# Kernel optimization log

Hardware: AMD Instinct MI355X
Metric: run time of the kernel (lower is better)

## Reference

```python
import jax, jax.numpy as jnp
import numpy as np

DIM = 1024
NUM_HEADS = 16
HEAD_DIM = DIM // NUM_HEADS
MAX_LEN = 2048
ROPE_BASE = 10000.0


def _rope_tables(n, d, base=ROPE_BASE):
    inv_freq = 1.0 / (base ** (np.arange(0, d, 2, dtype=np.float32) / d))  # [d/2]
    t = np.arange(n, dtype=np.float32)
    freqs = np.outer(t, inv_freq)  # [n, d/2]
    return jnp.asarray(np.cos(freqs)), jnp.asarray(np.sin(freqs))


def _apply_rotary(x, cos, sin):
    # x: [B, H, N, D]; pairs are consecutive elements (2i, 2i+1)
    xe = x[..., 0::2]
    xo = x[..., 1::2]
    # cos/sin: [N, D/2] -> broadcast over B, H
    oe = xe * cos - xo * sin
    oo = xe * sin + xo * cos
    return jnp.stack([oe, oo], axis=-1).reshape(x.shape)


def setup_inputs() -> dict:
    key = jax.random.key(0)
    ks = jax.random.split(key, 11)
    B, T, S = 4, 2048, 2048
    sc = 1.0 / np.sqrt(DIM)
    inp = {
        "query": jax.random.normal(ks[0], (B, T, DIM), jnp.float32),
        "key": jax.random.normal(ks[1], (B, S, DIM), jnp.float32),
        "value": jax.random.normal(ks[2], (B, S, DIM), jnp.float32),
        "Wq": jax.random.normal(ks[3], (DIM, DIM), jnp.float32) * sc,
        "bq": jnp.zeros((DIM,), jnp.float32),
        "Wk": jax.random.normal(ks[4], (DIM, DIM), jnp.float32) * sc,
        "bk": jnp.zeros((DIM,), jnp.float32),
        "Wv": jax.random.normal(ks[5], (DIM, DIM), jnp.float32) * sc,
        "bv": jnp.zeros((DIM,), jnp.float32),
        "Wo": jax.random.normal(ks[6], (DIM, DIM), jnp.float32) * sc,
        "bo": jnp.zeros((DIM,), jnp.float32),
    }
    return inp


def reference(query, key, value, Wq, bq, Wk, bk, Wv, bv, Wo, bo):
    B, T, C = query.shape
    S = key.shape[1]
    H, D = NUM_HEADS, HEAD_DIM
    scale = D ** -0.5

    q = (query @ Wq + bq).reshape(B, T, H, D).transpose(0, 2, 1, 3)  # [B,H,T,D]
    k = (key @ Wk + bk).reshape(B, S, H, D).transpose(0, 2, 1, 3)    # [B,H,S,D]
    v = (value @ Wv + bv).reshape(B, S, H, D).transpose(0, 2, 1, 3)  # [B,H,S,D]

    cos, sin = _rope_tables(max(T, S), D)
    q = _apply_rotary(q, cos[:T], sin[:T])
    k = _apply_rotary(k, cos[:S], sin[:S])

    scores = jnp.einsum("bhtd,bhsd->bhts", q, k) * scale  # [B,H,T,S]
    causal = jnp.tril(jnp.ones((T, S), bool))
    scores = jnp.where(causal[None, None], scores, -jnp.inf)
    att = jax.nn.softmax(scores, axis=-1)

    out = jnp.einsum("bhts,bhsd->bhtd", att, v)  # [B,H,T,D]
    out = out.transpose(0, 2, 1, 3).reshape(B, T, C)
    return out @ Wo + bo
```

## Files before the change

kernel.cpp:

```cpp
#include <hip/hip_runtime.h>
#include <cstdint>
#include <math.h>

typedef __bf16 bf16_t;
typedef __bf16 bf16x8 __attribute__((ext_vector_type(8)));
typedef float f32x4 __attribute__((ext_vector_type(4)));

#define MFMA16(a, b, c) __builtin_amdgcn_mfma_f32_16x16x32_bf16((a), (b), (c), 0, 0, 0)

static constexpr int BATCH = 4;
static constexpr int SEQ = 2048;
static constexpr int DIMC = 1024;
static constexpr int NH = 16;
static constexpr int HD = 64;

__device__ __forceinline__ void async_copy16(void* lds, const void* g) {
    __builtin_amdgcn_global_load_lds(
        (const __attribute__((address_space(1))) void*)g,
        (__attribute__((address_space(3))) void*)lds, 16, 0, 0);
}

__device__ __forceinline__ float fast_exp2(float x) {
#if __has_builtin(__builtin_amdgcn_exp2f)
    return __builtin_amdgcn_exp2f(x);
#else
    return __expf(x * 0.6931471805599453f);
#endif
}

__global__ __launch_bounds__(256) void cvt_bf16(const float* __restrict__ in,
                                                bf16_t* __restrict__ out) {
    const int i = blockIdx.x * 256 + threadIdx.x;
    const float4 f0 = ((const float4*)in)[i * 2];
    const float4 f1 = ((const float4*)in)[i * 2 + 1];
    bf16x8 v;
    v[0] = (bf16_t)f0.x; v[1] = (bf16_t)f0.y; v[2] = (bf16_t)f0.z; v[3] = (bf16_t)f0.w;
    v[4] = (bf16_t)f1.x; v[5] = (bf16_t)f1.y; v[6] = (bf16_t)f1.z; v[7] = (bf16_t)f1.w;
    ((bf16x8*)out)[i] = v;
}

__global__ __launch_bounds__(256) void transpose_cvt(const float* __restrict__ W0,
                                                     const float* __restrict__ W1,
                                                     const float* __restrict__ W2,
                                                     const float* __restrict__ W3,
                                                     bf16_t* __restrict__ out) {
    const float* Ws[4] = {W0, W1, W2, W3};
    const float* W = Ws[blockIdx.z];
    bf16_t* Wt = out + (size_t)blockIdx.z * DIMC * DIMC;
    __shared__ float tile[32][33];
    const int tx = threadIdx.x & 31;
    const int ty = threadIdx.x >> 5;
    const int x0 = blockIdx.x * 32;
    const int y0 = blockIdx.y * 32;
    #pragma unroll
    for (int j = ty; j < 32; j += 8)
        tile[j][tx] = W[(size_t)(y0 + j) * DIMC + x0 + tx];
    __syncthreads();
    #pragma unroll
    for (int j = ty; j < 32; j += 8)
        Wt[(size_t)(x0 + j) * DIMC + y0 + tx] = (bf16_t)tile[tx][j];
}

__global__ __launch_bounds__(256) void rope_tab(float* __restrict__ cosT, float* __restrict__ sinT) {
    const int idx = blockIdx.x * 256 + threadIdx.x;
    const int t = idx >> 5;
    const int p = idx & 31;
    const float inv = exp2f(-0.41524101186092029f * (float)p);
    const float ang = (float)t * inv;
    float s, c;
    sincosf(ang, &s, &c);
    cosT[idx] = c;
    sinT[idx] = s;
}

template <int MODE>
__global__ __launch_bounds__(256) void gemm_kernel(const bf16_t* __restrict__ A,
                                                   const bf16_t* __restrict__ Bt,
                                                   const float* __restrict__ bias,
                                                   void* __restrict__ outv,
                                                   const float* __restrict__ cosT,
                                                   const float* __restrict__ sinT) {
    constexpr int K = DIMC;
    __shared__ bf16_t As[128 * 32];
    __shared__ bf16_t Bs[128 * 32];
    const int tid = threadIdx.x;
    const int w = tid >> 6;
    const int lane = tid & 63;
    const int l15 = lane & 15;
    const int quad = lane >> 4;
    const int wr = w >> 1, wc = w & 1;
    const int row0 = blockIdx.y * 128, col0 = blockIdx.x * 128;
    f32x4 acc[4][4] = {};
    for (int kt = 0; kt < K / 32; ++kt) {
        const int k0 = kt * 32;
        __syncthreads();
        #pragma unroll
        for (int ci = 0; ci < 2; ++ci) {
            const int c = 2 * w + ci;
            async_copy16(&Bs[c * 512],
                         Bt + (size_t)(col0 + c * 16 + (lane >> 2)) * K + k0 + (lane & 3) * 8);
            async_copy16(&As[c * 512],
                         A + (size_t)(row0 + c * 16 + (lane >> 2)) * K + k0 + (lane & 3) * 8);
        }
        __syncthreads();
        bf16x8 af[4], bfr[4];
        #pragma unroll
        for (int mt = 0; mt < 4; ++mt)
            af[mt] = *(const bf16x8*)&As[(wr * 64 + mt * 16 + l15) * 32 + quad * 8];
        #pragma unroll
        for (int nt = 0; nt < 4; ++nt)
            bfr[nt] = *(const bf16x8*)&Bs[(wc * 64 + nt * 16 + l15) * 32 + quad * 8];
        #pragma unroll
        for (int mt = 0; mt < 4; ++mt)
            #pragma unroll
            for (int nt = 0; nt < 4; ++nt)
                acc[mt][nt] = MFMA16(af[mt], bfr[nt], acc[mt][nt]);
    }
    #pragma unroll
    for (int nt = 0; nt < 4; ++nt) {
        const int col = col0 + wc * 64 + nt * 16 + l15;
        const float bv = bias[col];
        #pragma unroll
        for (int mt = 0; mt < 4; ++mt) {
            #pragma unroll
            for (int r = 0; r < 4; ++r) {
                const int row = row0 + wr * 64 + mt * 16 + quad * 4 + r;
                float v = acc[mt][nt][r] + bv;
                if constexpr (MODE == 2) {
                    ((float*)outv)[(size_t)row * DIMC + col] = v;
                } else {
                    const int t = row & (SEQ - 1);
                    const int bb = row >> 11;
                    const int h = col >> 6;
                    const int d = col & 63;
                    float o = v;
                    if constexpr (MODE == 0) {
                        const int p = d >> 1;
                        const float cs = cosT[t * 32 + p];
                        const float sn = sinT[t * 32 + p];
                        const float partner = __shfl_xor(v, 1);
                        o = (d & 1) ? (partner * sn + v * cs) : (v * cs - partner * sn);
                    }
                    ((bf16_t*)outv)[(((size_t)bb * NH + h) * SEQ + t) * HD + d] = (bf16_t)o;
                }
            }
        }
    }
}

__global__ __launch_bounds__(256) void attn_kernel(const bf16_t* __restrict__ Qr,
                                                   const bf16_t* __restrict__ Kr,
                                                   const bf16_t* __restrict__ Vr,
                                                   bf16_t* __restrict__ O) {
    __shared__ bf16_t Ks[64 * 72];
    __shared__ bf16_t Vt[64 * 72];
    __shared__ bf16_t Ps[4][32 * 72];
    const int tid = threadIdx.x;
    const int w = tid >> 6;
    const int lane = tid & 63;
    const int l15 = lane & 15;
    const int quad = lane >> 4;
    const int bh = blockIdx.y;
    const int b = bh >> 4, h = bh & 15;
    const bf16_t* Qb = Qr + (size_t)bh * SEQ * HD;
    const bf16_t* Kb = Kr + (size_t)bh * SEQ * HD;
    const bf16_t* Vb = Vr + (size_t)bh * SEQ * HD;
    const float S2 = 0.18033688011112043f;

    bf16x8 ones;
    #pragma unroll
    for (int j8 = 0; j8 < 8; ++j8) ones[j8] = (bf16_t)1.0f;

    for (int half = 0; half < 2; ++half) {
        const int j = (half == 0) ? blockIdx.x : 15 - blockIdx.x;
        const int q0 = j * 128;
        bf16x8 qa[2][2];
        #pragma unroll
        for (int mg = 0; mg < 2; ++mg)
            #pragma unroll
            for (int kc = 0; kc < 2; ++kc)
                qa[mg][kc] = *(const bf16x8*)(Qb + (size_t)(q0 + mg * 64 + w * 16 + l15) * HD +
                                              kc * 32 + quad * 8);
        f32x4 acco[2][4] = {};
        f32x4 accl[2] = {};
        const int nIter = 2 * j + 2;
        for (int it = 0; it < nIter; ++it) {
            const int s0 = it * 64;
            __syncthreads();
            {
                const int s = tid >> 2, c4 = tid & 3;
                const bf16_t* src = Kb + (size_t)(s0 + s) * HD + c4 * 16;
                bf16x8 k0 = *(const bf16x8*)src;
                bf16x8 k1 = *(const bf16x8*)(src + 8);
                *(bf16x8*)&Ks[s * 72 + c4 * 16] = k0;
                *(bf16x8*)&Ks[s * 72 + c4 * 16 + 8] = k1;
            }
            #pragma unroll
            for (int cc = 0; cc < 2; ++cc) {
                const int d0 = w * 8 + cc * 32;
                const int s = lane;
                bf16x8 vv = *(const bf16x8*)(Vb + (size_t)(s0 + s) * HD + d0);
                #pragma unroll
                for (int j8 = 0; j8 < 8; ++j8) Vt[(d0 + j8) * 72 + s] = vv[j8];
            }
            __syncthreads();
            bf16x8 kb[4][2];
            #pragma unroll
            for (int nt = 0; nt < 4; ++nt) {
                kb[nt][0] = *(const bf16x8*)&Ks[(nt * 16 + l15) * 72 + quad * 8];
                kb[nt][1] = *(const bf16x8*)&Ks[(nt * 16 + l15) * 72 + 32 + quad * 8];
            }
            #pragma unroll
            for (int mg = 0; mg < 2; ++mg) {
                if (mg == 0 && it == 2 * j + 1) continue;
                f32x4 sc[4];
                #pragma unroll
                for (int nt = 0; nt < 4; ++nt) {
                    f32x4 z = {};
                    z = MFMA16(qa[mg][0], kb[nt][0], z);
                    z = MFMA16(qa[mg][1], kb[nt][1], z);
                    sc[nt] = z;
                }
                const bool diag = (it == 2 * j + mg);
                #pragma unroll
                for (int nt = 0; nt < 4; ++nt) {
                    #pragma unroll
                    for (int r = 0; r < 4; ++r) {
                        float v = sc[nt][r];
                        if (diag) {
                            const int lcol = nt * 16 + l15;
                            const int lrow = w * 16 + quad * 4 + r;
                            if (lcol > lrow) v = -INFINITY;
                        }
                        const float p = fast_exp2(S2 * v);
                        Ps[w][(mg * 16 + quad * 4 + r) * 72 + nt * 16 + l15] = (bf16_t)p;
                    }
                }
            }
            asm volatile("s_waitcnt lgkmcnt(0)" ::: "memory");
            bf16x8 vb[4][2];
            #pragma unroll
            for (int dt = 0; dt < 4; ++dt) {
                vb[dt][0] = *(const bf16x8*)&Vt[(dt * 16 + l15) * 72 + quad * 8];
                vb[dt][1] = *(const bf16x8*)&Vt[(dt * 16 + l15) * 72 + 32 + quad * 8];
            }
            #pragma unroll
            for (int mg = 0; mg < 2; ++mg) {
                if (mg == 0 && it == 2 * j + 1) continue;
                const bf16x8 pa0 = *(const bf16x8*)&Ps[w][(mg * 16 + l15) * 72 + quad * 8];
                const bf16x8 pa1 = *(const bf16x8*)&Ps[w][(mg * 16 + l15) * 72 + 32 + quad * 8];
                #pragma unroll
                for (int dt = 0; dt < 4; ++dt) {
                    acco[mg][dt] = MFMA16(pa0, vb[dt][0], acco[mg][dt]);
                    acco[mg][dt] = MFMA16(pa1, vb[dt][1], acco[mg][dt]);
                }
                accl[mg] = MFMA16(pa0, ones, accl[mg]);
                accl[mg] = MFMA16(pa1, ones, accl[mg]);
            }
        }
        #pragma unroll
        for (int mg = 0; mg < 2; ++mg) {
            #pragma unroll
            for (int r = 0; r < 4; ++r) {
                const float inv = 1.0f / accl[mg][r];
                const int trow = q0 + mg * 64 + w * 16 + quad * 4 + r;
                bf16_t* orow = O + ((size_t)(b * SEQ + trow)) * DIMC + h * HD;
                #pragma unroll
                for (int dt = 0; dt < 4; ++dt)
                    orow[dt * 16 + l15] = (bf16_t)(acco[mg][dt][r] * inv);
            }
        }
    }
}

extern "C" void kernel_launch(void* const* d_in, const int* in_sizes, int n_in,
                              void* d_out, int out_size, void* d_ws, size_t ws_size,
                              hipStream_t stream) {
    const float* query = (const float*)d_in[0];
    const float* key = (const float*)d_in[1];
    const float* value = (const float*)d_in[2];
    const float* Wq = (const float*)d_in[3];
    const float* bq = (const float*)d_in[4];
    const float* Wk = (const float*)d_in[5];
    const float* bk = (const float*)d_in[6];
    const float* Wv = (const float*)d_in[7];
    const float* bv = (const float*)d_in[8];
    const float* Wo = (const float*)d_in[9];
    const float* bo = (const float*)d_in[10];

    char* ws = (char*)d_ws;
    const size_t WT_BYTES = (size_t)DIMC * DIMC * sizeof(bf16_t);
    bf16_t* WqT = (bf16_t*)ws;
    bf16_t* WkT = WqT + (size_t)DIMC * DIMC;
    bf16_t* WvT = WqT + 2 * (size_t)DIMC * DIMC;
    bf16_t* WoT = WqT + 3 * (size_t)DIMC * DIMC;
    float* cosT = (float*)(ws + 4 * WT_BYTES);
    float* sinT = (float*)(ws + 4 * WT_BYTES + 262144);
    char* p = ws + 4 * WT_BYTES + 2 * 262144;
    const size_t ACT_BYTES = (size_t)BATCH * SEQ * DIMC * sizeof(bf16_t);
    bf16_t* Qr = (bf16_t*)(p);
    bf16_t* Kr = (bf16_t*)(p + ACT_BYTES);
    bf16_t* Vr = (bf16_t*)(p + 2 * ACT_BYTES);
    bf16_t* Ob = (bf16_t*)(p + 3 * ACT_BYTES);

    transpose_cvt<<<dim3(32, 32, 4), 256, 0, stream>>>(Wq, Wk, Wv, Wo, (bf16_t*)ws);
    rope_tab<<<dim3(256), 256, 0, stream>>>(cosT, sinT);

    const int cvt_blocks = (BATCH * SEQ * DIMC) / (8 * 256);
    dim3 gg(DIMC / 128, (BATCH * SEQ) / 128);

    cvt_bf16<<<dim3(cvt_blocks), 256, 0, stream>>>(query, Ob);
    gemm_kernel<0><<<gg, 256, 0, stream>>>(Ob, WqT, bq, Qr, cosT, sinT);
    cvt_bf16<<<dim3(cvt_blocks), 256, 0, stream>>>(key, Ob);
    gemm_kernel<0><<<gg, 256, 0, stream>>>(Ob, WkT, bk, Kr, cosT, sinT);
    cvt_bf16<<<dim3(cvt_blocks), 256, 0, stream>>>(value, Ob);
    gemm_kernel<1><<<gg, 256, 0, stream>>>(Ob, WvT, bv, Vr, cosT, sinT);

    attn_kernel<<<dim3(8, BATCH * NH), 256, 0, stream>>>(Qr, Kr, Vr, Ob);
    gemm_kernel<2><<<gg, 256, 0, stream>>>(Ob, WoT, bo, d_out, nullptr, nullptr);
}
```

Measured before the change: 374.9 us.

## Batch QKV projections, swizzle GEMM LDS, async K loads and MFMA-based V transpose

The three input conversions and three projection GEMMs are merged into single launches over a z grid dimension, so there are fewer launches and each wave is larger. GEMM LDS tiles use an XOR swizzle to cut bank conflicts on fragment reads. In attention, K tiles are loaded with async global-to-LDS copies into a swizzled unpadded buffer. V is transposed through an identity-matrix MFMA instead of scalar LDS scatter, and the score MFMA operands are swapped so P can be stored as packed 4-wide vectors. These changes trade more complex indexing and extra MFMA work for fewer launches and less LDS traffic.

Result: no change. 372.6 us (-0.6%).

```diff
diff --git a/kernel.cpp b/kernel.cpp
--- a/kernel.cpp
+++ b/kernel.cpp
@@ -4,6 +4,7 @@
 
 typedef __bf16 bf16_t;
 typedef __bf16 bf16x8 __attribute__((ext_vector_type(8)));
+typedef __bf16 bf16x4 __attribute__((ext_vector_type(4)));
 typedef float f32x4 __attribute__((ext_vector_type(4)));
 
 #define MFMA16(a, b, c) __builtin_amdgcn_mfma_f32_16x16x32_bf16((a), (b), (c), 0, 0, 0)
@@ -28,15 +29,19 @@
 #endif
 }
 
-__global__ __launch_bounds__(256) void cvt_bf16(const float* __restrict__ in,
-                                                bf16_t* __restrict__ out) {
+__global__ __launch_bounds__(256) void cvt3(const float* __restrict__ q,
+                                            const float* __restrict__ k,
+                                            const float* __restrict__ v,
+                                            bf16_t* __restrict__ out) {
+    const float* in = (blockIdx.y == 0) ? q : ((blockIdx.y == 1) ? k : v);
+    bf16_t* o = out + (size_t)blockIdx.y * BATCH * SEQ * DIMC;
     const int i = blockIdx.x * 256 + threadIdx.x;
     const float4 f0 = ((const float4*)in)[i * 2];
     const float4 f1 = ((const float4*)in)[i * 2 + 1];
-    bf16x8 v;
-    v[0] = (bf16_t)f0.x; v[1] = (bf16_t)f0.y; v[2] = (bf16_t)f0.z; v[3] = (bf16_t)f0.w;
-    v[4] = (bf16_t)f1.x; v[5] = (bf16_t)f1.y; v[6] = (bf16_t)f1.z; v[7] = (bf16_t)f1.w;
-    ((bf16x8*)out)[i] = v;
+    bf16x8 vv;
+    vv[0] = (bf16_t)f0.x; vv[1] = (bf16_t)f0.y; vv[2] = (bf16_t)f0.z; vv[3] = (bf16_t)f0.w;
+    vv[4] = (bf16_t)f1.x; vv[5] = (bf16_t)f1.y; vv[6] = (bf16_t)f1.z; vv[7] = (bf16_t)f1.w;
+    ((bf16x8*)o)[i] = vv;
 }
 
 __global__ __launch_bounds__(256) void transpose_cvt(const float* __restrict__ W0,
@@ -73,14 +78,89 @@
     sinT[idx] = s;
 }
 
-template <int MODE>
-__global__ __launch_bounds__(256) void gemm_kernel(const bf16_t* __restrict__ A,
-                                                   const bf16_t* __restrict__ Bt,
-                                                   const float* __restrict__ bias,
-                                                   void* __restrict__ outv,
-                                                   const float* __restrict__ cosT,
-                                                   const float* __restrict__ sinT) {
-    constexpr int K = DIMC;
+#define GEMM_KLOOP(A_, Bt_)                                                             \
+    f32x4 acc[4][4] = {};                                                               \
+    const int swW = ((lane >> 2) & 3) ^ ((lane >> 4) & 3);         \
+    const int rIn = lane >> 2;                                    \
+    const int gW = ((lane & 3) ^ swW) * 8;                        \
+    const int fR = (l15 & 3) ^ ((l15 >> 2) & 3);                    \
+    for (int kt = 0; kt < DIMC / 32; ++kt) {                                            \
+        const int k0 = kt * 32;                                                         \
+        __syncthreads();                                                                \
+        _Pragma("unroll") for (int ci = 0; ci < 2; ++ci) {                              \
+            const int c = 2 * w + ci;                                                   \
+            async_copy16(&Bs[c * 512], Bt_ + (size_t)(col0 + c * 16 + rIn) * DIMC + k0 + gW); \
+            async_copy16(&As[c * 512], A_ + (size_t)(row0 + c * 16 + rIn) * DIMC + k0 + gW);  \
+        }                                                                               \
+        __syncthreads();                                                                \
+        bf16x8 af[4], bfr[4];                                                           \
+        _Pragma("unroll") for (int mt = 0; mt < 4; ++mt)                                \
+            af[mt] = *(const bf16x8*)&As[(wr * 64 + mt * 16 + l15) * 32 + ((quad ^ fR) << 3)]; \
+        _Pragma("unroll") for (int nt = 0; nt < 4; ++nt)                                \
+            bfr[nt] = *(const bf16x8*)&Bs[(wc * 64 + nt * 16 + l15) * 32 + ((quad ^ fR) << 3)]; \
+        _Pragma("unroll") for (int mt = 0; mt < 4; ++mt)                                \
+            _Pragma("unroll") for (int nt = 0; nt < 4; ++nt)                            \
+                acc[mt][nt] = MFMA16(af[mt], bfr[nt], acc[mt][nt]);                     \
+    }
+
+__global__ __launch_bounds__(256) void gemm_qkv(const bf16_t* __restrict__ Cb,
+                                                const bf16_t* __restrict__ Wt3,
+                                                const float* __restrict__ bq,
+                                                const float* __restrict__ bk,
+                                                const float* __restrict__ bv,
+                                                bf16_t* __restrict__ Qr,
+                                                bf16_t* __restrict__ Kr,
+                                                bf16_t* __restrict__ Vr,
+                                                const float* __restrict__ cosT,
+                                                const float* __restrict__ sinT) {
+    __shared__ bf16_t As[128 * 32];
+    __shared__ bf16_t Bs[128 * 32];
+    const int z = blockIdx.z;
+    const bf16_t* A = Cb + (size_t)z * BATCH * SEQ * DIMC;
+    const bf16_t* Bt = Wt3 + (size_t)z * DIMC * DIMC;
+    const float* bias = (z == 0) ? bq : ((z == 1) ? bk : bv);
+    bf16_t* outp = (z == 0) ? Qr : ((z == 1) ? Kr : Vr);
+    const bool rope = (z < 2);
+    const int tid = threadIdx.x;
+    const int w = tid >> 6;
+    const int lane = tid & 63;
+    const int l15 = lane & 15;
+    const int quad = lane >> 4;
+    const int wr = w >> 1, wc = w & 1;
+    const int row0 = blockIdx.y * 128, col0 = blockIdx.x * 128;
+    GEMM_KLOOP(A, Bt)
+    #pragma unroll
+    for (int nt = 0; nt < 4; ++nt) {
+        const int col = col0 + wc * 64 + nt * 16 + l15;
+        const float bvl = bias[col];
+        const int h = col >> 6;
+        const int d = col & 63;
+        #pragma unroll
+        for (int mt = 0; mt < 4; ++mt) {
+            #pragma unroll
+            for (int r = 0; r < 4; ++r) {
+                const int row = row0 + wr * 64 + mt * 16 + quad * 4 + r;
+                const int t = row & (SEQ - 1);
+                const int bb = row >> 11;
+                float v = acc[mt][nt][r] + bvl;
+                float o = v;
+                if (rope) {
+                    const int p = d >> 1;
+                    const float cs = cosT[t * 32 + p];
+                    const float sn = sinT[t * 32 + p];
+                    const float partner = __shfl_xor(v, 1);
+                    o = (d & 1) ? (partner * sn + v * cs) : (v * cs - partner * sn);
+                }
+                outp[(((size_t)bb * NH + h) * SEQ + t) * HD + d] = (bf16_t)o;
+            }
+        }
+    }
+}
+
+__global__ __launch_bounds__(256) void gemm_o(const bf16_t* __restrict__ A,
+                                              const bf16_t* __restrict__ Bt,
+                                              const float* __restrict__ bias,
+                                              float* __restrict__ out) {
     __shared__ bf16_t As[128 * 32];
     __shared__ bf16_t Bs[128 * 32];
     const int tid = threadIdx.x;
@@ -90,59 +170,17 @@
     const int quad = lane >> 4;
     const int wr = w >> 1, wc = w & 1;
     const int row0 = blockIdx.y * 128, col0 = blockIdx.x * 128;
-    f32x4 acc[4][4] = {};
-    for (int kt = 0; kt < K / 32; ++kt) {
-        const int k0 = kt * 32;
-        __syncthreads();
-        #pragma unroll
-        for (int ci = 0; ci < 2; ++ci) {
-            const int c = 2 * w + ci;
-            async_copy16(&Bs[c * 512],
-                         Bt + (size_t)(col0 + c * 16 + (lane >> 2)) * K + k0 + (lane & 3) * 8);
-            async_copy16(&As[c * 512],
-                         A + (size_t)(row0 + c * 16 + (lane >> 2)) * K + k0 + (lane & 3) * 8);
-        }
-        __syncthreads();
-        bf16x8 af[4], bfr[4];
-        #pragma unroll
-        for (int mt = 0; mt < 4; ++mt)
-            af[mt] = *(const bf16x8*)&As[(wr * 64 + mt * 16 + l15) * 32 + quad * 8];
-        #pragma unroll
-        for (int nt = 0; nt < 4; ++nt)
-            bfr[nt] = *(const bf16x8*)&Bs[(wc * 64 + nt * 16 + l15) * 32 + quad * 8];
-        #pragma unroll
-        for (int mt = 0; mt < 4; ++mt)
-            #pragma unroll
-            for (int nt = 0; nt < 4; ++nt)
-                acc[mt][nt] = MFMA16(af[mt], bfr[nt], acc[mt][nt]);
-    }
+    GEMM_KLOOP(A, Bt)
     #pragma unroll
     for (int nt = 0; nt < 4; ++nt) {
         const int col = col0 + wc * 64 + nt * 16 + l15;
-        const float bv = bias[col];
+        const float bvl = bias[col];
         #pragma unroll
         for (int mt = 0; mt < 4; ++mt) {
             #pragma unroll
             for (int r = 0; r < 4; ++r) {
                 const int row = row0 + wr * 64 + mt * 16 + quad * 4 + r;
-                float v = acc[mt][nt][r] + bv;
-                if constexpr (MODE == 2) {
-                    ((float*)outv)[(size_t)row * DIMC + col] = v;
-                } else {
-                    const int t = row & (SEQ - 1);
-                    const int bb = row >> 11;
-                    const int h = col >> 6;
-                    const int d = col & 63;
-                    float o = v;
-                    if constexpr (MODE == 0) {
-                        const int p = d >> 1;
-                        const float cs = cosT[t * 32 + p];
-                        const float sn = sinT[t * 32 + p];
-                        const float partner = __shfl_xor(v, 1);
-                        o = (d & 1) ? (partner * sn + v * cs) : (v * cs - partner * sn);
-                    }
-                    ((bf16_t*)outv)[(((size_t)bb * NH + h) * SEQ + t) * HD + d] = (bf16_t)o;
-                }
+                out[(size_t)row * DIMC + col] = acc[mt][nt][r] + bvl;
             }
         }
     }
@@ -152,7 +190,7 @@
                                                    const bf16_t* __restrict__ Kr,
                                                    const bf16_t* __restrict__ Vr,
                                                    bf16_t* __restrict__ O) {
-    __shared__ bf16_t Ks[64 * 72];
+    __shared__ bf16_t Ks[64 * 64];
     __shared__ bf16_t Vt[64 * 72];
     __shared__ bf16_t Ps[4][32 * 72];
     const int tid = threadIdx.x;
@@ -170,6 +208,16 @@
     bf16x8 ones;
     #pragma unroll
     for (int j8 = 0; j8 < 8; ++j8) ones[j8] = (bf16_t)1.0f;
+    bf16x8 idB[2];
+    #pragma unroll
+    for (int ch = 0; ch < 2; ++ch)
+        #pragma unroll
+        for (int j8 = 0; j8 < 8; ++j8)
+            idB[ch][j8] = (quad * 8 + j8 == ch * 16 + l15) ? (bf16_t)1.0f : (bf16_t)0.0f;
+
+    const int sIn = lane >> 3;
+    const int gK = ((lane & 7) ^ sIn) * 8;
+    const int fK = (l15 & 7);
 
     for (int half = 0; half < 2; ++half) {
         const int j = (half == 0) ? blockIdx.x : 15 - blockIdx.x;
@@ -187,63 +235,59 @@
         for (int it = 0; it < nIter; ++it) {
             const int s0 = it * 64;
             __syncthreads();
+            #pragma unroll
+            for (int ci = 0; ci < 2; ++ci) {
+                const int c = 2 * w + ci;
+                async_copy16(&Ks[c * 512], Kb + (size_t)(s0 + c * 8 + sIn) * HD + gK);
+            }
             {
-                const int s = tid >> 2, c4 = tid & 3;
-                const bf16_t* src = Kb + (size_t)(s0 + s) * HD + c4 * 16;
-                bf16x8 k0 = *(const bf16x8*)src;
-                bf16x8 k1 = *(const bf16x8*)(src + 8);
-                *(bf16x8*)&Ks[s * 72 + c4 * 16] = k0;
-                *(bf16x8*)&Ks[s * 72 + c4 * 16 + 8] = k1;
-            }
-            #pragma unroll
-            for (int cc = 0; cc < 2; ++cc) {
-                const int d0 = w * 8 + cc * 32;
-                const int s = lane;
-                bf16x8 vv = *(const bf16x8*)(Vb + (size_t)(s0 + s) * HD + d0);
-                #pragma unroll
-                for (int j8 = 0; j8 < 8; ++j8) Vt[(d0 + j8) * 72 + s] = vv[j8];
+                const bf16_t* vsrc = Vb + (size_t)(s0 + w * 16 + l15) * HD + quad * 8;
+                bf16x8 av0 = *(const bf16x8*)(vsrc);
+                bf16x8 av1 = *(const bf16x8*)(vsrc + 32);
+                #pragma unroll
+                for (int c = 0; c < 4; ++c) {
+                    f32x4 zz = {};
+                    f32x4 tv = MFMA16((c < 2) ? av0 : av1, idB[c & 1], zz);
+                    bf16x4 pk;
+                    #pragma unroll
+                    for (int r = 0; r < 4; ++r) pk[r] = (bf16_t)tv[r];
+                    *(bf16x4*)&Vt[(c * 16 + l15) * 72 + w * 16 + quad * 4] = pk;
+                }
             }
             __syncthreads();
             bf16x8 kb[4][2];
             #pragma unroll
-            for (int nt = 0; nt < 4; ++nt) {
-                kb[nt][0] = *(const bf16x8*)&Ks[(nt * 16 + l15) * 72 + quad * 8];
-                kb[nt][1] = *(const bf16x8*)&Ks[(nt * 16 + l15) * 72 + 32 + quad * 8];
-            }
+            for (int mt = 0; mt < 4; ++mt)
+                #pragma unroll
+                for (int kc = 0; kc < 2; ++kc)
+                    kb[mt][kc] = *(const bf16x8*)&Ks[(mt * 16 + l15) * 64 +
+                                                     (((kc * 4 + quad) ^ fK) << 3)];
             #pragma unroll
             for (int mg = 0; mg < 2; ++mg) {
                 if (mg == 0 && it == 2 * j + 1) continue;
-                f32x4 sc[4];
-                #pragma unroll
-                for (int nt = 0; nt < 4; ++nt) {
+                const bool diag = (it == 2 * j + mg);
+                #pragma unroll
+                for (int mt = 0; mt < 4; ++mt) {
                     f32x4 z = {};
-                    z = MFMA16(qa[mg][0], kb[nt][0], z);
-                    z = MFMA16(qa[mg][1], kb[nt][1], z);
-                    sc[nt] = z;
-                }
-                const bool diag = (it == 2 * j + mg);
-                #pragma unroll
-                for (int nt = 0; nt < 4; ++nt) {
+                    z = MFMA16(kb[mt][0], qa[mg][0], z);
+                    z = MFMA16(kb[mt][1], qa[mg][1], z);
+                    bf16x4 pk;
                     #pragma unroll
                     for (int r = 0; r < 4; ++r) {
-                        float v = sc[nt][r];
-                        if (diag) {
-                            const int lcol = nt * 16 + l15;
-                            const int lrow = w * 16 + quad * 4 + r;
-                            if (lcol > lrow) v = -INFINITY;
-                        }
-                        const float p = fast_exp2(S2 * v);
-                        Ps[w][(mg * 16 + quad * 4 + r) * 72 + nt * 16 + l15] = (bf16_t)p;
+                        float v = z[r];
+                        if (diag && (mt * 16 + quad * 4 + r > w * 16 + l15)) v = -INFINITY;
+                        pk[r] = (bf16_t)fast_exp2(S2 * v);
                     }
+                    *(bf16x4*)&Ps[w][(mg * 16 + l15) * 72 + mt * 16 + quad * 4] = pk;
                 }
             }
             asm volatile("s_waitcnt lgkmcnt(0)" ::: "memory");
             bf16x8 vb[4][2];
             #pragma unroll
-            for (int dt = 0; dt < 4; ++dt) {
-                vb[dt][0] = *(const bf16x8*)&Vt[(dt * 16 + l15) * 72 + quad * 8];
-                vb[dt][1] = *(const bf16x8*)&Vt[(dt * 16 + l15) * 72 + 32 + quad * 8];
-            }
+            for (int dt = 0; dt < 4; ++dt)
+                #pragma unroll
+                for (int kc = 0; kc < 2; ++kc)
+                    vb[dt][kc] = *(const bf16x8*)&Vt[(dt * 16 + l15) * 72 + kc * 32 + quad * 8];
             #pragma unroll
             for (int mg = 0; mg < 2; ++mg) {
                 if (mg == 0 && it == 2 * j + 1) continue;
@@ -290,32 +334,22 @@
 
     char* ws = (char*)d_ws;
     const size_t WT_BYTES = (size_t)DIMC * DIMC * sizeof(bf16_t);
-    bf16_t* WqT = (bf16_t*)ws;
-    bf16_t* WkT = WqT + (size_t)DIMC * DIMC;
-    bf16_t* WvT = WqT + 2 * (size_t)DIMC * DIMC;
-    bf16_t* WoT = WqT + 3 * (size_t)DIMC * DIMC;
+    const size_t ACT_BYTES = (size_t)BATCH * SEQ * DIMC * sizeof(bf16_t);
+    bf16_t* WT = (bf16_t*)ws;
+    bf16_t* WoT = WT + 3 * (size_t)DIMC * DIMC;
     float* cosT = (float*)(ws + 4 * WT_BYTES);
     float* sinT = (float*)(ws + 4 * WT_BYTES + 262144);
-    char* p = ws + 4 * WT_BYTES + 2 * 262144;
-    const size_t ACT_BYTES = (size_t)BATCH * SEQ * DIMC * sizeof(bf16_t);
-    bf16_t* Qr = (bf16_t*)(p);
-    bf16_t* Kr = (bf16_t*)(p + ACT_BYTES);
-    bf16_t* Vr = (bf16_t*)(p + 2 * ACT_BYTES);
-    bf16_t* Ob = (bf16_t*)(p + 3 * ACT_BYTES);
-
-    transpose_cvt<<<dim3(32, 32, 4), 256, 0, stream>>>(Wq, Wk, Wv, Wo, (bf16_t*)ws);
+    bf16_t* Cb = (bf16_t*)(ws + 4 * WT_BYTES + 2 * 262144);
+    bf16_t* Qr = (bf16_t*)((char*)Cb + 3 * ACT_BYTES);
+    bf16_t* Kr = (bf16_t*)((char*)Cb + 4 * ACT_BYTES);
+    bf16_t* Vr = (bf16_t*)((char*)Cb + 5 * ACT_BYTES);
+    bf16_t* Ob = Cb;
+
+    transpose_cvt<<<dim3(32, 32, 4), 256, 0, stream>>>(Wq, Wk, Wv, Wo, WT);
     rope_tab<<<dim3(256), 256, 0, stream>>>(cosT, sinT);
-
-    const int cvt_blocks = (BATCH * SEQ * DIMC) / (8 * 256);
-    dim3 gg(DIMC / 128, (BATCH * SEQ) / 128);
-
-    cvt_bf16<<<dim3(cvt_blocks), 256, 0, stream>>>(query, Ob);
-    gemm_kernel<0><<<gg, 256, 0, stream>>>(Ob, WqT, bq, Qr, cosT, sinT);
-    cvt_bf16<<<dim3(cvt_blocks), 256, 0, stream>>>(key, Ob);
-    gemm_kernel<0><<<gg, 256, 0, stream>>>(Ob, WkT, bk, Kr, cosT, sinT);
-    cvt_bf16<<<dim3(cvt_blocks), 256, 0, stream>>>(value, Ob);
-    gemm_kernel<1><<<gg, 256, 0, stream>>>(Ob, WvT, bv, Vr, cosT, sinT);
-
+    cvt3<<<dim3(4096, 3), 256, 0, stream>>>(query, key, value, Cb);
+    gemm_qkv<<<dim3(DIMC / 128, (BATCH * SEQ) / 128, 3), 256, 0, stream>>>(
+        Cb, WT, bq, bk, bv, Qr, Kr, Vr, cosT, sinT);
     attn_kernel<<<dim3(8, BATCH * NH), 256, 0, stream>>>(Qr, Kr, Vr, Ob);
-    gemm_kernel<2><<<gg, 256, 0, stream>>>(Ob, WoT, bo, d_out, nullptr, nullptr);
-}
+    gemm_o<<<dim3(DIMC / 128, (BATCH * SEQ) / 128), 256, 0, stream>>>(Ob, WoT, bo, (float*)d_out);
+}
```
